# Kernel tuning notes

Measured on AMD Instinct MI355X. Metric: run time of the kernel, lower is better.

The kernel has to match this reference:

```python
import jax, jax.numpy as jnp
import numpy as np

N_CELL, N_GENE, D, E = 100000, 20000, 128, 1000000


def setup_inputs() -> dict:
    key = jax.random.key(0)
    ks = jax.random.split(key, 16)
    return {
        "cell_z": jax.random.normal(ks[0], (N_CELL, D), jnp.float32),
        "gene_z": jax.random.normal(ks[1], (N_GENE, D), jnp.float32),
        "W_gene": jax.random.normal(ks[2], (D, D), jnp.float32) / np.sqrt(D),
        "b_gene": jax.random.normal(ks[3], (D,), jnp.float32) * 0.01,
        "cell_scale": jax.random.normal(ks[4], (N_CELL,), jnp.float32),
        "cell_bias": jax.random.normal(ks[5], (N_CELL,), jnp.float32),
        "cell_std": jax.random.uniform(ks[6], (N_CELL,), jnp.float32, 0.1, 1.0),
        "gene_scale": jax.random.normal(ks[7], (N_GENE,), jnp.float32),
        "gene_bias": jax.random.normal(ks[8], (N_GENE,), jnp.float32),
        "gene_std": jax.random.uniform(ks[9], (N_GENE,), jnp.float32, 0.1, 1.0),
        "src_idx": jax.random.randint(ks[10], (E,), 0, N_CELL, jnp.int32),
        "dst_idx": jax.random.randint(ks[11], (E,), 0, N_GENE, jnp.int32),
        "cell_n_id": jax.random.randint(ks[12], (N_CELL,), 0, N_CELL, jnp.int32),
        "gene_n_id": jax.random.randint(ks[13], (N_GENE,), 0, N_GENE, jnp.int32),
    }


def reference(cell_z, gene_z, W_gene, b_gene,
              cell_scale, cell_bias, cell_std,
              gene_scale, gene_bias, gene_std,
              src_idx, dst_idx, cell_n_id, gene_n_id):
    # Relation projection: 'cell' -> Identity, 'gene' -> Linear + LeakyReLU.
    # Project per-node then gather (mathematically identical to the original
    # gather-then-project since projection is pointwise per node).
    gene_proj = jax.nn.leaky_relu(gene_z @ W_gene + b_gene)  # [N_GENE, D]
    u = cell_z[src_idx]            # [E, D] gather of src node embeddings
    v = gene_proj[dst_idx]         # [E, D] gather of projected dst embeddings

    # Per-edge scale/bias/std lookups via global node ids (n_id[edge_index]).
    sid = cell_n_id[src_idx]       # [E]
    did = gene_n_id[dst_idx]       # [E]
    s_sc, s_b, s_sd = cell_scale[sid], cell_bias[sid], cell_std[sid]
    d_sc, d_b, d_sd = gene_scale[did], gene_bias[did], gene_std[did]

    dot = jnp.sum(u * v, axis=-1)  # [E]
    loc = dot * s_sc * d_sc + s_b + d_b
    std = s_sd * d_sd
    return jnp.stack([loc, std])   # [2, E]
```

## Files before the change

kernel.cpp:

```cpp
#include <hip/hip_runtime.h>

#define N_CELL 100000
#define N_GENE 20000
#define DIM    128
#define N_EDGE 1000000

#define NS_STRIPE 20
#define NTILE     40
#define NBLK_SORT 977

#define NB_WCAST 8
#define NB_CTAB  391
#define NB_GTAB  79
#define NB_MISC  (NB_WCAST + NB_CTAB + NB_GTAB)

#define NB_PROJ  625
#define NB_HIST  977
#define NB_CAST  6250
#define NB_PREP  (NB_PROJ + NB_HIST + NB_CAST)

#define NGRP     125000
#define NB_EDGE  7813

typedef float f32x4 __attribute__((ext_vector_type(4)));

__device__ inline unsigned short f2bf(float f) {
    unsigned u = __float_as_uint(f);
    u += 0x7fffu + ((u >> 16) & 1u);
    return (unsigned short)(u >> 16);
}

__device__ inline void dot2(float& acc, unsigned a, unsigned b) {
    asm("v_dot2_f32_bf16 %0, %1, %2, %0" : "+v"(acc) : "v"(a), "v"(b));
}

__device__ inline int tile_of(int s, int d) {
    const int ss = (int)(((unsigned long long)s * 429497ULL) >> 31);
    const int ds = (d >= 10000) ? 1 : 0;
    return ds * NS_STRIPE + ss;
}

__device__ inline unsigned pack_sd(int s, int d) {
    return ((unsigned)s << 15) | (unsigned)d;
}

__device__ inline float lrelu(float v) { return v > 0.f ? v : 0.01f * v; }

__global__ __launch_bounds__(256) void misc_kernel(
    const float* __restrict__ W,
    ushort* __restrict__ Wbt,
    const int*   __restrict__ cell_n_id,
    const int*   __restrict__ gene_n_id,
    const float* __restrict__ cell_scale,
    const float* __restrict__ cell_bias,
    const float* __restrict__ cell_std,
    const float* __restrict__ gene_scale,
    const float* __restrict__ gene_bias,
    const float* __restrict__ gene_std,
    float4* __restrict__ cell_p4,
    float4* __restrict__ gene_p4)
{
    const int tid = threadIdx.x;
    int blk = blockIdx.x;

    if (blk < NB_WCAST) {
        const int t   = blk * 256 + tid;
        const int col = t >> 4;
        const int k8  = t & 15;
        unsigned short w[8];
        #pragma unroll
        for (int j = 0; j < 8; ++j)
            w[j] = f2bf(W[(k8 * 8 + j) * DIM + col]);
        uint4 o;
        o.x = (unsigned)w[0] | ((unsigned)w[1] << 16);
        o.y = (unsigned)w[2] | ((unsigned)w[3] << 16);
        o.z = (unsigned)w[4] | ((unsigned)w[5] << 16);
        o.w = (unsigned)w[6] | ((unsigned)w[7] << 16);
        ((uint4*)Wbt)[t] = o;
        return;
    }
    blk -= NB_WCAST;

    if (blk < NB_CTAB) {
        const int c = blk * 256 + tid;
        if (c < N_CELL) {
            const int id = cell_n_id[c];
            cell_p4[c] = make_float4(cell_scale[id], cell_bias[id],
                                     cell_std[id], 0.f);
        }
        return;
    }
    blk -= NB_CTAB;

    const int g = blk * 256 + tid;
    if (g < N_GENE) {
        const int id = gene_n_id[g];
        gene_p4[g] = make_float4(gene_scale[id], gene_bias[id],
                                 gene_std[id], 0.f);
    }
}

__global__ __launch_bounds__(256) void prep_fused(
    const float* __restrict__ gene_z,
    const float* __restrict__ b,
    const ushort* __restrict__ Wbt,
    ushort* __restrict__ gene_projb,
    const float* __restrict__ cell_z,
    ushort4* __restrict__ cell_zb4,
    const int* __restrict__ src_idx,
    const int* __restrict__ dst_idx,
    int* __restrict__ counts)
{
    __shared__ ushort zb[32 * DIM];
    __shared__ uint4  wl[2048];

    const int tid = threadIdx.x;
    int blk = blockIdx.x;

    if (blk < NB_PROJ) {
        const uint4* wg = (const uint4*)Wbt;
        #pragma unroll
        for (int i = 0; i < 8; ++i) {
            const int u = i * 256 + tid;
            const int c = u >> 4, j = u & 15;
            wl[(c << 4) | (j ^ (c & 15))] = wg[u];
        }
        const int row0 = blk * 32;
        const f32x4* Z4 = (const f32x4*)(gene_z + (long)row0 * DIM);
        #pragma unroll
        for (int i = 0; i < 4; ++i) {
            const int idx = i * 256 + tid;
            const f32x4 v = Z4[idx];
            ushort4 o;
            o.x = f2bf(v.x); o.y = f2bf(v.y); o.z = f2bf(v.z); o.w = f2bf(v.w);
            ((ushort4*)zb)[idx] = o;
        }
        __syncthreads();

        const int cg = tid & 31;
        const int rg = tid >> 5;

        const float4 bb = ((const float4*)b)[cg];
        float acc[4][4];
        #pragma unroll
        for (int r = 0; r < 4; ++r) {
            acc[r][0] = bb.x; acc[r][1] = bb.y;
            acc[r][2] = bb.z; acc[r][3] = bb.w;
        }

        const uint4* zr = (const uint4*)zb;
        #pragma unroll 4
        for (int k8 = 0; k8 < 16; ++k8) {
            uint4 z[4], w[4];
            #pragma unroll
            for (int r = 0; r < 4; ++r)
                z[r] = zr[(rg * 4 + r) * 16 + k8];
            #pragma unroll
            for (int c = 0; c < 4; ++c) {
                const int col = cg * 4 + c;
                w[c] = wl[(col << 4) | (k8 ^ (col & 15))];
            }
            #pragma unroll
            for (int r = 0; r < 4; ++r)
                #pragma unroll
                for (int c = 0; c < 4; ++c) {
                    dot2(acc[r][c], z[r].x, w[c].x);
                    dot2(acc[r][c], z[r].y, w[c].y);
                    dot2(acc[r][c], z[r].z, w[c].z);
                    dot2(acc[r][c], z[r].w, w[c].w);
                }
        }

        #pragma unroll
        for (int r = 0; r < 4; ++r) {
            ushort4 o;
            o.x = f2bf(lrelu(acc[r][0]));
            o.y = f2bf(lrelu(acc[r][1]));
            o.z = f2bf(lrelu(acc[r][2]));
            o.w = f2bf(lrelu(acc[r][3]));
            *(ushort4*)(gene_projb + (long)(row0 + rg * 4 + r) * DIM + cg * 4) = o;
        }
        return;
    }
    blk -= NB_PROJ;

    if (blk < NB_HIST) {
        int* lcnt = (int*)zb;
        if (tid < NTILE) lcnt[tid] = 0;
        __syncthreads();
        #pragma unroll
        for (int q = 0; q < 4; ++q) {
            const int e = blk * 1024 + q * 256 + tid;
            if (e < N_EDGE) {
                const int t = tile_of(src_idx[e], dst_idx[e]);
                atomicAdd(&lcnt[t], 1);
            }
        }
        __syncthreads();
        if (tid < NTILE) counts[tid * NBLK_SORT + blk] = lcnt[tid];
        return;
    }
    blk -= NB_HIST;

    const f32x4* in4 = (const f32x4*)cell_z;
    const int base = blk * 512 + tid;
    const f32x4 v0 = in4[base];
    const f32x4 v1 = in4[base + 256];
    ushort4 o0, o1;
    o0.x = f2bf(v0.x); o0.y = f2bf(v0.y); o0.z = f2bf(v0.z); o0.w = f2bf(v0.w);
    o1.x = f2bf(v1.x); o1.y = f2bf(v1.y); o1.z = f2bf(v1.z); o1.w = f2bf(v1.w);
    cell_zb4[base]       = o0;
    cell_zb4[base + 256] = o1;
}

__global__ __launch_bounds__(256) void scanA_kernel(
    int* __restrict__ counts, int* __restrict__ totals)
{
    __shared__ int sd[256];
    const int t   = blockIdx.x;
    const int tid = threadIdx.x;
    int carry = 0;
    for (int c = 0; c < 4; ++c) {
        const int idx = c * 256 + tid;
        const int val = (idx < NBLK_SORT) ? counts[t * NBLK_SORT + idx] : 0;
        sd[tid] = val;
        __syncthreads();
        #pragma unroll
        for (int off = 1; off < 256; off <<= 1) {
            const int tmp = (tid >= off) ? sd[tid - off] : 0;
            __syncthreads();
            sd[tid] += tmp;
            __syncthreads();
        }
        const int incl = sd[tid];
        const int ctot = sd[255];
        if (idx < NBLK_SORT) counts[t * NBLK_SORT + idx] = carry + incl - val;
        carry += ctot;
        __syncthreads();
    }
    if (tid == 0) totals[t] = carry;
}

__global__ __launch_bounds__(256) void scatter_kernel(
    const int* __restrict__ src_idx,
    const int* __restrict__ dst_idx,
    const int* __restrict__ counts,
    const int* __restrict__ totals,
    unsigned* __restrict__ sorted_p,
    int*      __restrict__ rank)
{
    __shared__ int lcnt[NTILE];
    __shared__ int sbase[NTILE];
    __shared__ int lbase[NTILE];
    const int tid = threadIdx.x;
    const int blk = blockIdx.x;
    if (tid < NTILE) lcnt[tid] = 0;
    __syncthreads();

    int ts[4], rs[4], ss[4], ds[4];
    #pragma unroll
    for (int c = 0; c < 4; ++c) {
        const int e = blk * 1024 + c * 256 + tid;
        if (e < N_EDGE) {
            ss[c] = src_idx[e];
            ds[c] = dst_idx[e];
            ts[c] = tile_of(ss[c], ds[c]);
            rs[c] = atomicAdd(&lcnt[ts[c]], 1);
        } else { ts[c] = -1; rs[c] = 0; ss[c] = 0; ds[c] = 0; }
    }
    __syncthreads();
    if (tid == 0) {
        int s = 0;
        for (int i = 0; i < NTILE; ++i) { sbase[i] = s; s += totals[i]; }
    }
    __syncthreads();
    if (tid < NTILE) lbase[tid] = sbase[tid] + counts[tid * NBLK_SORT + blk];
    __syncthreads();

    #pragma unroll
    for (int c = 0; c < 4; ++c) {
        const int e = blk * 1024 + c * 256 + tid;
        if (ts[c] >= 0) {
            const int pos = lbase[ts[c]] + rs[c];
            sorted_p[pos] = pack_sd(ss[c], ds[c]);
            rank[e] = pos;
        }
    }
}

__global__ __launch_bounds__(256) void edge_sorted_kernel(
    const ushort* __restrict__ cell_zb,
    const ushort* __restrict__ gene_projb,
    const unsigned* __restrict__ sorted_p,
    const float4* __restrict__ cell_p4,
    const float4* __restrict__ gene_p4,
    float2* __restrict__ res)
{
    const int wg  = blockIdx.x;
    const int xcd = wg & 7;
    const int sub = wg >> 3;
    const int q = NB_EDGE / 8, r = NB_EDGE % 8;
    const int swz = ((xcd < r) ? xcd * (q + 1) : r * (q + 1) + (xcd - r) * q) + sub;

    const int tid  = threadIdx.x;
    const int lane = tid & 15;
    const int grp  = swz * 16 + (tid >> 4);
    if (grp >= NGRP) return;

    const uint4 pa = ((const uint4*)sorted_p)[grp * 2];
    const uint4 pb = ((const uint4*)sorted_p)[grp * 2 + 1];
    const int s0 = (int)(pa.x >> 15), d0 = (int)(pa.x & 0x7fffu);
    const int s1 = (int)(pa.y >> 15), d1 = (int)(pa.y & 0x7fffu);
    const int s2 = (int)(pa.z >> 15), d2 = (int)(pa.z & 0x7fffu);
    const int s3 = (int)(pa.w >> 15), d3 = (int)(pa.w & 0x7fffu);
    const int s4 = (int)(pb.x >> 15), d4 = (int)(pb.x & 0x7fffu);
    const int s5 = (int)(pb.y >> 15), d5 = (int)(pb.y & 0x7fffu);
    const int s6 = (int)(pb.z >> 15), d6 = (int)(pb.z & 0x7fffu);
    const int s7 = (int)(pb.w >> 15), d7 = (int)(pb.w & 0x7fffu);

    const uint4 a0 = ((const uint4*)(cell_zb + (long)s0 * DIM))[lane];
    const uint4 a1 = ((const uint4*)(cell_zb + (long)s1 * DIM))[lane];
    const uint4 a2 = ((const uint4*)(cell_zb + (long)s2 * DIM))[lane];
    const uint4 a3 = ((const uint4*)(cell_zb + (long)s3 * DIM))[lane];
    const uint4 a4 = ((const uint4*)(cell_zb + (long)s4 * DIM))[lane];
    const uint4 a5 = ((const uint4*)(cell_zb + (long)s5 * DIM))[lane];
    const uint4 a6 = ((const uint4*)(cell_zb + (long)s6 * DIM))[lane];
    const uint4 a7 = ((const uint4*)(cell_zb + (long)s7 * DIM))[lane];
    const uint4 v0 = ((const uint4*)(gene_projb + (long)d0 * DIM))[lane];
    const uint4 v1 = ((const uint4*)(gene_projb + (long)d1 * DIM))[lane];
    const uint4 v2 = ((const uint4*)(gene_projb + (long)d2 * DIM))[lane];
    const uint4 v3 = ((const uint4*)(gene_projb + (long)d3 * DIM))[lane];
    const uint4 v4 = ((const uint4*)(gene_projb + (long)d4 * DIM))[lane];
    const uint4 v5 = ((const uint4*)(gene_projb + (long)d5 * DIM))[lane];
    const uint4 v6 = ((const uint4*)(gene_projb + (long)d6 * DIM))[lane];
    const uint4 v7 = ((const uint4*)(gene_projb + (long)d7 * DIM))[lane];

    float t0 = 0.f, t1 = 0.f, t2 = 0.f, t3 = 0.f;
    float t4 = 0.f, t5 = 0.f, t6 = 0.f, t7 = 0.f;
    #define D4(acc, aa, vv)                 \
        dot2(acc, aa.x, vv.x); dot2(acc, aa.y, vv.y); \
        dot2(acc, aa.z, vv.z); dot2(acc, aa.w, vv.w);
    D4(t0, a0, v0) D4(t1, a1, v1) D4(t2, a2, v2) D4(t3, a3, v3)
    D4(t4, a4, v4) D4(t5, a5, v5) D4(t6, a6, v6) D4(t7, a7, v7)
    #undef D4

    #define RED(d)                 \
        d += __shfl_xor(d, 1);     \
        d += __shfl_xor(d, 2);     \
        d += __shfl_xor(d, 4);     \
        d += __shfl_xor(d, 8);
    RED(t0) RED(t1) RED(t2) RED(t3) RED(t4) RED(t5) RED(t6) RED(t7)
    #undef RED

    if (lane < 8) {
        #define SEL(x0,x1,x2,x3,x4,x5,x6,x7)                                   \
            ((lane & 4) ? ((lane & 2) ? ((lane & 1) ? x7 : x6)                 \
                                      : ((lane & 1) ? x5 : x4))                \
                        : ((lane & 2) ? ((lane & 1) ? x3 : x2)                 \
                                      : ((lane & 1) ? x1 : x0)))
        const float dj  = SEL(t0, t1, t2, t3, t4, t5, t6, t7);
        const int   sj  = SEL(s0, s1, s2, s3, s4, s5, s6, s7);
        const int   djx = SEL(d0, d1, d2, d3, d4, d5, d6, d7);
        #undef SEL
        const float4 cs = cell_p4[sj];
        const float4 gs = gene_p4[djx];
        res[grp * 8 + lane] =
            make_float2(dj * cs.x * gs.x + cs.y + gs.y, cs.z * gs.z);
    }
}

__global__ __launch_bounds__(256) void fixup_kernel(
    const int*    __restrict__ rank,
    const float2* __restrict__ res,
    float* __restrict__ out)
{
    const int e0 = (blockIdx.x * 256 + threadIdx.x) * 4;
    if (e0 >= N_EDGE) return;
    const int4 r4 = *(const int4*)(rank + e0);
    const float2 r0 = res[r4.x];
    const float2 r1 = res[r4.y];
    const float2 r2 = res[r4.z];
    const float2 r3 = res[r4.w];
    *(float4*)(out + e0)          = make_float4(r0.x, r1.x, r2.x, r3.x);
    *(float4*)(out + N_EDGE + e0) = make_float4(r0.y, r1.y, r2.y, r3.y);
}

__global__ __launch_bounds__(256) void edge_fallback(
    const float*  __restrict__ cell_z,
    const ushort* __restrict__ gene_projb,
    const int*   __restrict__ src_idx,
    const int*   __restrict__ dst_idx,
    const int*   __restrict__ cell_n_id,
    const int*   __restrict__ gene_n_id,
    const float* __restrict__ cell_scale,
    const float* __restrict__ cell_bias,
    const float* __restrict__ cell_std,
    const float* __restrict__ gene_scale,
    const float* __restrict__ gene_bias,
    const float* __restrict__ gene_std,
    float* __restrict__ out)
{
    const int tid  = threadIdx.x;
    const int lane = tid & 15;
    const int e    = blockIdx.x * 16 + (tid >> 4);

    const int s = src_idx[e];
    const int d = dst_idx[e];
    const float4* up = (const float4*)(cell_z + (long)s * DIM);
    const float4 ua = up[2 * lane], ub = up[2 * lane + 1];
    const uint4  v  = ((const uint4*)(gene_projb + (long)d * DIM))[lane];

    float dot = 0.f;
    dot = fmaf(ua.x, __uint_as_float(v.x << 16), dot);
    dot = fmaf(ua.y, __uint_as_float(v.x & 0xffff0000u), dot);
    dot = fmaf(ua.z, __uint_as_float(v.y << 16), dot);
    dot = fmaf(ua.w, __uint_as_float(v.y & 0xffff0000u), dot);
    dot = fmaf(ub.x, __uint_as_float(v.z << 16), dot);
    dot = fmaf(ub.y, __uint_as_float(v.z & 0xffff0000u), dot);
    dot = fmaf(ub.z, __uint_as_float(v.w << 16), dot);
    dot = fmaf(ub.w, __uint_as_float(v.w & 0xffff0000u), dot);

    dot += __shfl_xor(dot, 1);
    dot += __shfl_xor(dot, 2);
    dot += __shfl_xor(dot, 4);
    dot += __shfl_xor(dot, 8);

    if (lane == 0) {
        const int sid = cell_n_id[s];
        const int did = gene_n_id[d];
        out[e]          = dot * cell_scale[sid] * gene_scale[did]
                        + cell_bias[sid] + gene_bias[did];
        out[N_EDGE + e] = cell_std[sid] * gene_std[did];
    }
}

extern "C" void kernel_launch(void* const* d_in, const int* in_sizes, int n_in,
                              void* d_out, int out_size, void* d_ws, size_t ws_size,
                              hipStream_t stream) {
    const float* cell_z     = (const float*)d_in[0];
    const float* gene_z     = (const float*)d_in[1];
    const float* W_gene     = (const float*)d_in[2];
    const float* b_gene     = (const float*)d_in[3];
    const float* cell_scale = (const float*)d_in[4];
    const float* cell_bias  = (const float*)d_in[5];
    const float* cell_std   = (const float*)d_in[6];
    const float* gene_scale = (const float*)d_in[7];
    const float* gene_bias  = (const float*)d_in[8];
    const float* gene_std   = (const float*)d_in[9];
    const int*   src_idx    = (const int*)d_in[10];
    const int*   dst_idx    = (const int*)d_in[11];
    const int*   cell_n_id  = (const int*)d_in[12];
    const int*   gene_n_id  = (const int*)d_in[13];

    char* ws = (char*)d_ws;
    size_t off = 0;
    ushort* gene_projb = (ushort*)(ws + off); off += (size_t)N_GENE * DIM * 2;
    ushort* Wbt        = (ushort*)(ws + off); off += (size_t)DIM * DIM * 2;
    const size_t min_need = off;
    ushort* cell_zb    = (ushort*)(ws + off); off += (size_t)N_CELL * DIM * 2;
    float4* cell_p4    = (float4*)(ws + off); off += (size_t)N_CELL * 16;
    float4* gene_p4    = (float4*)(ws + off); off += (size_t)N_GENE * 16;
    unsigned* sorted_p = (unsigned*)(ws + off); off += (size_t)N_EDGE * 4;
    int*    rank       = (int*)(ws + off);    off += (size_t)N_EDGE * 4;
    float2* res        = (float2*)(ws + off); off += (size_t)N_EDGE * 8;
    int*    counts     = (int*)(ws + off);    off += (size_t)NTILE * NBLK_SORT * 4;
    int*    totals     = (int*)(ws + off);    off += 256;

    float* out = (float*)d_out;

    if (ws_size < off) {
        (void)min_need;
        misc_kernel<<<NB_WCAST, 256, 0, stream>>>(
            W_gene, Wbt, cell_n_id, gene_n_id,
            cell_scale, cell_bias, cell_std,
            gene_scale, gene_bias, gene_std, nullptr, nullptr);
        prep_fused<<<NB_PROJ, 256, 0, stream>>>(
            gene_z, b_gene, Wbt, gene_projb,
            cell_z, nullptr, src_idx, dst_idx, nullptr);
        edge_fallback<<<N_EDGE / 16, 256, 0, stream>>>(
            cell_z, gene_projb, src_idx, dst_idx, cell_n_id, gene_n_id,
            cell_scale, cell_bias, cell_std,
            gene_scale, gene_bias, gene_std, out);
        return;
    }

    misc_kernel<<<NB_MISC, 256, 0, stream>>>(
        W_gene, Wbt, cell_n_id, gene_n_id,
        cell_scale, cell_bias, cell_std,
        gene_scale, gene_bias, gene_std, cell_p4, gene_p4);
    prep_fused<<<NB_PREP, 256, 0, stream>>>(
        gene_z, b_gene, Wbt, gene_projb,
        cell_z, (ushort4*)cell_zb, src_idx, dst_idx, counts);
    scanA_kernel<<<NTILE, 256, 0, stream>>>(counts, totals);
    scatter_kernel<<<NBLK_SORT, 256, 0, stream>>>(
        src_idx, dst_idx, counts, totals, sorted_p, rank);
    edge_sorted_kernel<<<NB_EDGE, 256, 0, stream>>>(
        cell_zb, gene_projb, sorted_p, cell_p4, gene_p4, res);
    fixup_kernel<<<(N_EDGE / 4 + 255) / 256, 256, 0, stream>>>(rank, res, out);
}
```

Before: 85.84 us.

## Regroup prep kernels, fuse scatter with projection, shrink edges per group

The histogram and the cell bf16 cast move into the first prep kernel alongside the W cast and the parameter tables, and the cell cast now uses nontemporal loads and stores. The gene projection is merged with the scatter into a second kernel that runs after the scan, which removes one launch and lets projection overlap with the scatter. The edge kernel now handles 4 edges per 16-lane group instead of 8, doubling the block count to expose more parallelism at the cost of less memory-level parallelism per thread. The launch count drops from six to five.

```diff
diff --git a/kernel.cpp b/kernel.cpp
--- a/kernel.cpp
+++ b/kernel.cpp
@@ -10,19 +10,17 @@
 #define NBLK_SORT 977
 
 #define NB_WCAST 8
+#define NB_HIST  977
 #define NB_CTAB  391
 #define NB_GTAB  79
-#define NB_MISC  (NB_WCAST + NB_CTAB + NB_GTAB)
+#define NB_CAST  6250
+#define NB_PREP1 (NB_WCAST + NB_HIST + NB_CTAB + NB_GTAB + NB_CAST)
 
 #define NB_PROJ  625
-#define NB_HIST  977
-#define NB_CAST  6250
-#define NB_PREP  (NB_PROJ + NB_HIST + NB_CAST)
-
-#define NGRP     125000
-#define NB_EDGE  7813
-
-typedef float f32x4 __attribute__((ext_vector_type(4)));
+#define NB_PREP2 (NB_PROJ + NBLK_SORT)
+
+typedef float          f32x4 __attribute__((ext_vector_type(4)));
+typedef unsigned short u16x4 __attribute__((ext_vector_type(4)));
 
 __device__ inline unsigned short f2bf(float f) {
     unsigned u = __float_as_uint(f);
@@ -46,9 +44,12 @@
 
 __device__ inline float lrelu(float v) { return v > 0.f ? v : 0.01f * v; }
 
-__global__ __launch_bounds__(256) void misc_kernel(
+__global__ __launch_bounds__(256) void prep1_kernel(
     const float* __restrict__ W,
     ushort* __restrict__ Wbt,
+    const int*   __restrict__ src_idx,
+    const int*   __restrict__ dst_idx,
+    int* __restrict__ counts,
     const int*   __restrict__ cell_n_id,
     const int*   __restrict__ gene_n_id,
     const float* __restrict__ cell_scale,
@@ -58,8 +59,12 @@
     const float* __restrict__ gene_bias,
     const float* __restrict__ gene_std,
     float4* __restrict__ cell_p4,
-    float4* __restrict__ gene_p4)
-{
+    float4* __restrict__ gene_p4,
+    const float* __restrict__ cell_z,
+    ushort* __restrict__ cell_zb)
+{
+    __shared__ int lcnt[NTILE];
+
     const int tid = threadIdx.x;
     int blk = blockIdx.x;
 
@@ -81,6 +86,23 @@
     }
     blk -= NB_WCAST;
 
+    if (blk < NB_HIST) {
+        if (tid < NTILE) lcnt[tid] = 0;
+        __syncthreads();
+        #pragma unroll
+        for (int q = 0; q < 4; ++q) {
+            const int e = blk * 1024 + q * 256 + tid;
+            if (e < N_EDGE) {
+                const int t = tile_of(src_idx[e], dst_idx[e]);
+                atomicAdd(&lcnt[t], 1);
+            }
+        }
+        __syncthreads();
+        if (tid < NTILE) counts[tid * NBLK_SORT + blk] = lcnt[tid];
+        return;
+    }
+    blk -= NB_HIST;
+
     if (blk < NB_CTAB) {
         const int c = blk * 256 + tid;
         if (c < N_CELL) {
@@ -92,24 +114,68 @@
     }
     blk -= NB_CTAB;
 
-    const int g = blk * 256 + tid;
-    if (g < N_GENE) {
-        const int id = gene_n_id[g];
-        gene_p4[g] = make_float4(gene_scale[id], gene_bias[id],
-                                 gene_std[id], 0.f);
-    }
-}
-
-__global__ __launch_bounds__(256) void prep_fused(
+    if (blk < NB_GTAB) {
+        const int g = blk * 256 + tid;
+        if (g < N_GENE) {
+            const int id = gene_n_id[g];
+            gene_p4[g] = make_float4(gene_scale[id], gene_bias[id],
+                                     gene_std[id], 0.f);
+        }
+        return;
+    }
+    blk -= NB_GTAB;
+
+    const f32x4* in4 = (const f32x4*)cell_z;
+    u16x4* out4 = (u16x4*)cell_zb;
+    const int base = blk * 512 + tid;
+    const f32x4 v0 = __builtin_nontemporal_load(in4 + base);
+    const f32x4 v1 = __builtin_nontemporal_load(in4 + base + 256);
+    u16x4 o0, o1;
+    o0.x = f2bf(v0.x); o0.y = f2bf(v0.y); o0.z = f2bf(v0.z); o0.w = f2bf(v0.w);
+    o1.x = f2bf(v1.x); o1.y = f2bf(v1.y); o1.z = f2bf(v1.z); o1.w = f2bf(v1.w);
+    __builtin_nontemporal_store(o0, out4 + base);
+    __builtin_nontemporal_store(o1, out4 + base + 256);
+}
+
+__global__ __launch_bounds__(256) void scanA_kernel(
+    int* __restrict__ counts, int* __restrict__ totals)
+{
+    __shared__ int sd[256];
+    const int t   = blockIdx.x;
+    const int tid = threadIdx.x;
+    int carry = 0;
+    for (int c = 0; c < 4; ++c) {
+        const int idx = c * 256 + tid;
+        const int val = (idx < NBLK_SORT) ? counts[t * NBLK_SORT + idx] : 0;
+        sd[tid] = val;
+        __syncthreads();
+        #pragma unroll
+        for (int off = 1; off < 256; off <<= 1) {
+            const int tmp = (tid >= off) ? sd[tid - off] : 0;
+            __syncthreads();
+            sd[tid] += tmp;
+            __syncthreads();
+        }
+        const int incl = sd[tid];
+        const int ctot = sd[255];
+        if (idx < NBLK_SORT) counts[t * NBLK_SORT + idx] = carry + incl - val;
+        carry += ctot;
+        __syncthreads();
+    }
+    if (tid == 0) totals[t] = carry;
+}
+
+__global__ __launch_bounds__(256) void prep2_kernel(
     const float* __restrict__ gene_z,
     const float* __restrict__ b,
     const ushort* __restrict__ Wbt,
     ushort* __restrict__ gene_projb,
-    const float* __restrict__ cell_z,
-    ushort4* __restrict__ cell_zb4,
     const int* __restrict__ src_idx,
     const int* __restrict__ dst_idx,
-    int* __restrict__ counts)
+    const int* __restrict__ counts,
+    const int* __restrict__ totals,
+    unsigned* __restrict__ sorted_p,
+    int*      __restrict__ rank)
 {
     __shared__ ushort zb[32 * DIM];
     __shared__ uint4  wl[2048];
@@ -184,76 +250,9 @@
     }
     blk -= NB_PROJ;
 
-    if (blk < NB_HIST) {
-        int* lcnt = (int*)zb;
-        if (tid < NTILE) lcnt[tid] = 0;
-        __syncthreads();
-        #pragma unroll
-        for (int q = 0; q < 4; ++q) {
-            const int e = blk * 1024 + q * 256 + tid;
-            if (e < N_EDGE) {
-                const int t = tile_of(src_idx[e], dst_idx[e]);
-                atomicAdd(&lcnt[t], 1);
-            }
-        }
-        __syncthreads();
-        if (tid < NTILE) counts[tid * NBLK_SORT + blk] = lcnt[tid];
-        return;
-    }
-    blk -= NB_HIST;
-
-    const f32x4* in4 = (const f32x4*)cell_z;
-    const int base = blk * 512 + tid;
-    const f32x4 v0 = in4[base];
-    const f32x4 v1 = in4[base + 256];
-    ushort4 o0, o1;
-    o0.x = f2bf(v0.x); o0.y = f2bf(v0.y); o0.z = f2bf(v0.z); o0.w = f2bf(v0.w);
-    o1.x = f2bf(v1.x); o1.y = f2bf(v1.y); o1.z = f2bf(v1.z); o1.w = f2bf(v1.w);
-    cell_zb4[base]       = o0;
-    cell_zb4[base + 256] = o1;
-}
-
-__global__ __launch_bounds__(256) void scanA_kernel(
-    int* __restrict__ counts, int* __restrict__ totals)
-{
-    __shared__ int sd[256];
-    const int t   = blockIdx.x;
-    const int tid = threadIdx.x;
-    int carry = 0;
-    for (int c = 0; c < 4; ++c) {
-        const int idx = c * 256 + tid;
-        const int val = (idx < NBLK_SORT) ? counts[t * NBLK_SORT + idx] : 0;
-        sd[tid] = val;
-        __syncthreads();
-        #pragma unroll
-        for (int off = 1; off < 256; off <<= 1) {
-            const int tmp = (tid >= off) ? sd[tid - off] : 0;
-            __syncthreads();
-            sd[tid] += tmp;
-            __syncthreads();
-        }
-        const int incl = sd[tid];
-        const int ctot = sd[255];
-        if (idx < NBLK_SORT) counts[t * NBLK_SORT + idx] = carry + incl - val;
-        carry += ctot;
-        __syncthreads();
-    }
-    if (tid == 0) totals[t] = carry;
-}
-
-__global__ __launch_bounds__(256) void scatter_kernel(
-    const int* __restrict__ src_idx,
-    const int* __restrict__ dst_idx,
-    const int* __restrict__ counts,
-    const int* __restrict__ totals,
-    unsigned* __restrict__ sorted_p,
-    int*      __restrict__ rank)
-{
-    __shared__ int lcnt[NTILE];
-    __shared__ int sbase[NTILE];
-    __shared__ int lbase[NTILE];
-    const int tid = threadIdx.x;
-    const int blk = blockIdx.x;
+    int* lcnt  = (int*)zb;
+    int* sbase = (int*)zb + 64;
+    int* lbase = (int*)zb + 128;
     if (tid < NTILE) lcnt[tid] = 0;
     __syncthreads();
 
@@ -299,72 +298,56 @@
     const int wg  = blockIdx.x;
     const int xcd = wg & 7;
     const int sub = wg >> 3;
-    const int q = NB_EDGE / 8, r = NB_EDGE % 8;
+    const int q = 15625 / 8, r = 15625 % 8;
     const int swz = ((xcd < r) ? xcd * (q + 1) : r * (q + 1) + (xcd - r) * q) + sub;
 
     const int tid  = threadIdx.x;
     const int lane = tid & 15;
     const int grp  = swz * 16 + (tid >> 4);
-    if (grp >= NGRP) return;
-
-    const uint4 pa = ((const uint4*)sorted_p)[grp * 2];
-    const uint4 pb = ((const uint4*)sorted_p)[grp * 2 + 1];
-    const int s0 = (int)(pa.x >> 15), d0 = (int)(pa.x & 0x7fffu);
-    const int s1 = (int)(pa.y >> 15), d1 = (int)(pa.y & 0x7fffu);
-    const int s2 = (int)(pa.z >> 15), d2 = (int)(pa.z & 0x7fffu);
-    const int s3 = (int)(pa.w >> 15), d3 = (int)(pa.w & 0x7fffu);
-    const int s4 = (int)(pb.x >> 15), d4 = (int)(pb.x & 0x7fffu);
-    const int s5 = (int)(pb.y >> 15), d5 = (int)(pb.y & 0x7fffu);
-    const int s6 = (int)(pb.z >> 15), d6 = (int)(pb.z & 0x7fffu);
-    const int s7 = (int)(pb.w >> 15), d7 = (int)(pb.w & 0x7fffu);
+
+    const uint4 p = ((const uint4*)sorted_p)[grp];
+    const int s0 = (int)(p.x >> 15), d0 = (int)(p.x & 0x7fffu);
+    const int s1 = (int)(p.y >> 15), d1 = (int)(p.y & 0x7fffu);
+    const int s2 = (int)(p.z >> 15), d2 = (int)(p.z & 0x7fffu);
+    const int s3 = (int)(p.w >> 15), d3 = (int)(p.w & 0x7fffu);
 
     const uint4 a0 = ((const uint4*)(cell_zb + (long)s0 * DIM))[lane];
     const uint4 a1 = ((const uint4*)(cell_zb + (long)s1 * DIM))[lane];
     const uint4 a2 = ((const uint4*)(cell_zb + (long)s2 * DIM))[lane];
     const uint4 a3 = ((const uint4*)(cell_zb + (long)s3 * DIM))[lane];
-    const uint4 a4 = ((const uint4*)(cell_zb + (long)s4 * DIM))[lane];
-    const uint4 a5 = ((const uint4*)(cell_zb + (long)s5 * DIM))[lane];
-    const uint4 a6 = ((const uint4*)(cell_zb + (long)s6 * DIM))[lane];
-    const uint4 a7 = ((const uint4*)(cell_zb + (long)s7 * DIM))[lane];
     const uint4 v0 = ((const uint4*)(gene_projb + (long)d0 * DIM))[lane];
     const uint4 v1 = ((const uint4*)(gene_projb + (long)d1 * DIM))[lane];
     const uint4 v2 = ((const uint4*)(gene_projb + (long)d2 * DIM))[lane];
     const uint4 v3 = ((const uint4*)(gene_projb + (long)d3 * DIM))[lane];
-    const uint4 v4 = ((const uint4*)(gene_projb + (long)d4 * DIM))[lane];
-    const uint4 v5 = ((const uint4*)(gene_projb + (long)d5 * DIM))[lane];
-    const uint4 v6 = ((const uint4*)(gene_projb + (long)d6 * DIM))[lane];
-    const uint4 v7 = ((const uint4*)(gene_projb + (long)d7 * DIM))[lane];
-
-    float t0 = 0.f, t1 = 0.f, t2 = 0.f, t3 = 0.f;
-    float t4 = 0.f, t5 = 0.f, t6 = 0.f, t7 = 0.f;
-    #define D4(acc, aa, vv)                 \
-        dot2(acc, aa.x, vv.x); dot2(acc, aa.y, vv.y); \
-        dot2(acc, aa.z, vv.z); dot2(acc, aa.w, vv.w);
-    D4(t0, a0, v0) D4(t1, a1, v1) D4(t2, a2, v2) D4(t3, a3, v3)
-    D4(t4, a4, v4) D4(t5, a5, v5) D4(t6, a6, v6) D4(t7, a7, v7)
-    #undef D4
+
+    float dot0 = 0.f, dot1 = 0.f, dot2v = 0.f, dot3 = 0.f;
+    dot2(dot0, a0.x, v0.x); dot2(dot0, a0.y, v0.y);
+    dot2(dot0, a0.z, v0.z); dot2(dot0, a0.w, v0.w);
+    dot2(dot1, a1.x, v1.x); dot2(dot1, a1.y, v1.y);
+    dot2(dot1, a1.z, v1.z); dot2(dot1, a1.w, v1.w);
+    dot2(dot2v, a2.x, v2.x); dot2(dot2v, a2.y, v2.y);
+    dot2(dot2v, a2.z, v2.z); dot2(dot2v, a2.w, v2.w);
+    dot2(dot3, a3.x, v3.x); dot2(dot3, a3.y, v3.y);
+    dot2(dot3, a3.z, v3.z); dot2(dot3, a3.w, v3.w);
 
     #define RED(d)                 \
         d += __shfl_xor(d, 1);     \
         d += __shfl_xor(d, 2);     \
         d += __shfl_xor(d, 4);     \
         d += __shfl_xor(d, 8);
-    RED(t0) RED(t1) RED(t2) RED(t3) RED(t4) RED(t5) RED(t6) RED(t7)
+    RED(dot0) RED(dot1) RED(dot2v) RED(dot3)
     #undef RED
 
-    if (lane < 8) {
-        #define SEL(x0,x1,x2,x3,x4,x5,x6,x7)                                   \
-            ((lane & 4) ? ((lane & 2) ? ((lane & 1) ? x7 : x6)                 \
-                                      : ((lane & 1) ? x5 : x4))                \
-                        : ((lane & 2) ? ((lane & 1) ? x3 : x2)                 \
-                                      : ((lane & 1) ? x1 : x0)))
-        const float dj  = SEL(t0, t1, t2, t3, t4, t5, t6, t7);
-        const int   sj  = SEL(s0, s1, s2, s3, s4, s5, s6, s7);
-        const int   djx = SEL(d0, d1, d2, d3, d4, d5, d6, d7);
-        #undef SEL
+    if (lane < 4) {
+        const float dj = (lane & 2) ? ((lane & 1) ? dot3 : dot2v)
+                                    : ((lane & 1) ? dot1 : dot0);
+        const int sj   = (lane & 2) ? ((lane & 1) ? s3 : s2)
+                                    : ((lane & 1) ? s1 : s0);
+        const int djx  = (lane & 2) ? ((lane & 1) ? d3 : d2)
+                                    : ((lane & 1) ? d1 : d0);
         const float4 cs = cell_p4[sj];
         const float4 gs = gene_p4[djx];
-        res[grp * 8 + lane] =
+        res[grp * 4 + lane] =
             make_float2(dj * cs.x * gs.x + cs.y + gs.y, cs.z * gs.z);
     }
 }
@@ -456,7 +439,6 @@
     size_t off = 0;
     ushort* gene_projb = (ushort*)(ws + off); off += (size_t)N_GENE * DIM * 2;
     ushort* Wbt        = (ushort*)(ws + off); off += (size_t)DIM * DIM * 2;
-    const size_t min_need = off;
     ushort* cell_zb    = (ushort*)(ws + off); off += (size_t)N_CELL * DIM * 2;
     float4* cell_p4    = (float4*)(ws + off); off += (size_t)N_CELL * 16;
     float4* gene_p4    = (float4*)(ws + off); off += (size_t)N_GENE * 16;
@@ -469,14 +451,15 @@
     float* out = (float*)d_out;
 
     if (ws_size < off) {
-        (void)min_need;
-        misc_kernel<<<NB_WCAST, 256, 0, stream>>>(
-            W_gene, Wbt, cell_n_id, gene_n_id,
+        prep1_kernel<<<NB_WCAST, 256, 0, stream>>>(
+            W_gene, Wbt, src_idx, dst_idx, nullptr,
+            cell_n_id, gene_n_id,
             cell_scale, cell_bias, cell_std,
-            gene_scale, gene_bias, gene_std, nullptr, nullptr);
-        prep_fused<<<NB_PROJ, 256, 0, stream>>>(
+            gene_scale, gene_bias, gene_std,
+            nullptr, nullptr, cell_z, nullptr);
+        prep2_kernel<<<NB_PROJ, 256, 0, stream>>>(
             gene_z, b_gene, Wbt, gene_projb,
-            cell_z, nullptr, src_idx, dst_idx, nullptr);
+            src_idx, dst_idx, nullptr, nullptr, nullptr, nullptr);
         edge_fallback<<<N_EDGE / 16, 256, 0, stream>>>(
             cell_z, gene_projb, src_idx, dst_idx, cell_n_id, gene_n_id,
             cell_scale, cell_bias, cell_std,
@@ -484,17 +467,17 @@
         return;
     }
 
-    misc_kernel<<<NB_MISC, 256, 0, stream>>>(
-        W_gene, Wbt, cell_n_id, gene_n_id,
+    prep1_kernel<<<NB_PREP1, 256, 0, stream>>>(
+        W_gene, Wbt, src_idx, dst_idx, counts,
+        cell_n_id, gene_n_id,
         cell_scale, cell_bias, cell_std,
-        gene_scale, gene_bias, gene_std, cell_p4, gene_p4);
-    prep_fused<<<NB_PREP, 256, 0, stream>>>(
+        gene_scale, gene_bias, gene_std,
+        cell_p4, gene_p4, cell_z, cell_zb);
+    scanA_kernel<<<NTILE, 256, 0, stream>>>(counts, totals);
+    prep2_kernel<<<NB_PREP2, 256, 0, stream>>>(
         gene_z, b_gene, Wbt, gene_projb,
-        cell_z, (ushort4*)cell_zb, src_idx, dst_idx, counts);
-    scanA_kernel<<<NTILE, 256, 0, stream>>>(counts, totals);
-    scatter_kernel<<<NBLK_SORT, 256, 0, stream>>>(
         src_idx, dst_idx, counts, totals, sorted_p, rank);
-    edge_sorted_kernel<<<NB_EDGE, 256, 0, stream>>>(
+    edge_sorted_kernel<<<N_EDGE / 64, 256, 0, stream>>>(
         cell_zb, gene_projb, sorted_p, cell_p4, gene_p4, res);
     fixup_kernel<<<(N_EDGE / 4 + 255) / 256, 256, 0, stream>>>(rank, res, out);
 }
```

After: 86.50 us. No clear change (+0.8%).
